# Kernel optimization log

Measured on AMD Instinct MI355X. Metric: run time of the kernel, lower is better.

The kernel has to match this reference:

```python
import jax, jax.numpy as jnp
import numpy as np
from jax import lax

BATCH, CH, SEQ, D_MODEL = 4, 8, 1024, 512
D_STATE, D_CONV, EXPAND = 16, 4, 2
D_INNER = EXPAND * D_MODEL
DT_RANK = (D_MODEL + 15) // 16  # math.ceil(d_model / 16) as in mamba_ssm


def _silu(v):
    return v * jax.nn.sigmoid(v)


def setup_inputs() -> dict:
    key = jax.random.key(0)
    ks = jax.random.split(key, 8)
    s = lambda fan: 1.0 / np.sqrt(fan)
    x = jax.random.normal(ks[0], (BATCH, CH, SEQ, D_MODEL), jnp.float32)
    W_in = jax.random.normal(ks[1], (2 * D_INNER, D_MODEL), jnp.float32) * s(D_MODEL)
    conv_w = jax.random.normal(ks[2], (D_INNER, D_CONV), jnp.float32) * s(D_CONV)
    conv_b = jnp.zeros((D_INNER,), jnp.float32)
    W_xproj = jax.random.normal(ks[3], (DT_RANK + 2 * D_STATE, D_INNER), jnp.float32) * s(D_INNER)
    W_dt = jax.random.normal(ks[4], (D_INNER, DT_RANK), jnp.float32) * s(DT_RANK)
    # dt bias ~ inverse-softplus of dt in [1e-3, 0.1] (mamba init)
    dt0 = jnp.exp(jax.random.uniform(ks[5], (D_INNER,), jnp.float32) * (np.log(0.1) - np.log(1e-3)) + np.log(1e-3))
    b_dt = dt0 + jnp.log(-jnp.expm1(-dt0))
    A_log = jnp.log(jnp.broadcast_to(jnp.arange(1, D_STATE + 1, dtype=jnp.float32), (D_INNER, D_STATE)))
    D = jnp.ones((D_INNER,), jnp.float32)
    W_out = jax.random.normal(ks[6], (D_MODEL, D_INNER), jnp.float32) * s(D_INNER)
    return {"x": x, "W_in": W_in, "conv_w": conv_w, "conv_b": conv_b,
            "W_xproj": W_xproj, "W_dt": W_dt, "b_dt": b_dt,
            "A_log": A_log, "D": D, "W_out": W_out}


def _mamba(u, W_in, conv_w, conv_b, W_xproj, W_dt, b_dt, A_log, D, W_out):
    # u: (B, L, d_model)
    Bn, L, _ = u.shape
    xz = u @ W_in.T                                  # (B, L, 2*d_inner)
    xs, z = jnp.split(xz, 2, axis=-1)
    # depthwise causal conv1d, padding=d_conv-1, truncated to L
    xt = jnp.pad(xs.transpose(0, 2, 1), ((0, 0), (0, 0), (D_CONV - 1, 0)))  # (B, d_inner, L+pad)
    xc = lax.conv_general_dilated(xt, conv_w[:, None, :], (1,), 'VALID',
                                  feature_group_count=D_INNER,
                                  dimension_numbers=('NCH', 'OIH', 'NCH'))   # (B, d_inner, L)
    xs = _silu((xc + conv_b[None, :, None]).transpose(0, 2, 1))              # (B, L, d_inner)
    x_dbl = xs @ W_xproj.T                           # (B, L, dt_rank + 2*d_state)
    dt_in = x_dbl[..., :DT_RANK]
    Bm = x_dbl[..., DT_RANK:DT_RANK + D_STATE]       # (B, L, d_state)
    Cm = x_dbl[..., DT_RANK + D_STATE:]              # (B, L, d_state)
    dt = jax.nn.softplus(dt_in @ W_dt.T + b_dt)      # (B, L, d_inner)
    A = -jnp.exp(A_log)                              # (d_inner, d_state)

    def step(h, inp):
        dt_t, B_t, C_t, x_t = inp                    # (B,di), (B,ds), (B,ds), (B,di)
        dA = jnp.exp(dt_t[..., None] * A)            # (B, di, ds)
        h = dA * h + (dt_t * x_t)[..., None] * B_t[:, None, :]
        y = jnp.einsum('bds,bs->bd', h, C_t)
        return h, y

    h0 = jnp.zeros((Bn, D_INNER, D_STATE), xs.dtype)
    xsL = (dt.transpose(1, 0, 2), Bm.transpose(1, 0, 2), Cm.transpose(1, 0, 2), xs.transpose(1, 0, 2))
    _, ys = lax.scan(step, h0, xsL)                  # ys: (L, B, d_inner)
    y = ys.transpose(1, 0, 2) + xs * D
    y = y * _silu(z)
    return y @ W_out.T                               # (B, L, d_model)


def reference(x, W_in, conv_w, conv_b, W_xproj, W_dt, b_dt, A_log, D, W_out):
    b, c, L, dm = x.shape
    # shared Mamba weights over channels -> fold channel into batch (== per-channel loop)
    u = x.reshape(b * c, L, dm)
    out = _mamba(u, W_in, conv_w, conv_b, W_xproj, W_dt, b_dt, A_log, D, W_out)
    return out.reshape(b, c, L, dm)
```

## Files before the change

kernel.cpp:

```cpp
#include <hip/hip_runtime.h>
#include <hip/hip_bf16.h>
#include <math.h>

#define BATCHN   4
#define CHN      8
#define SEQ      1024
#define DMODEL   512
#define DSTATE   16
#define DCONV    4
#define DINNER   1024
#define DTRANK   32
#define NROWS    32768
#define XD       64
#define NBC      32

#define GCH   16
#define CLEN  (SEQ / GCH)
#define SUB   32
#define PSLOT 17

#define CSPL  8
#define CTS   (SEQ / CSPL)

enum { EPI_NONE = 0, EPI_GATE = 1 };

__device__ __forceinline__ float siluf(float v) {
    return v / (1.0f + expf(-v));
}
__device__ __forceinline__ float softplus_fast(float v) {
    return (v > 20.0f) ? v : __logf(1.0f + __expf(v));
}

typedef short short8 __attribute__((ext_vector_type(8)));
typedef float floatx4 __attribute__((ext_vector_type(4)));

__device__ __forceinline__ unsigned short f2bf_rne(float f) {
    unsigned int u = __float_as_uint(f);
    u += 0x7fffu + ((u >> 16) & 1u);
    return (unsigned short)(u >> 16);
}
__device__ __forceinline__ float bf2f(unsigned short h) {
    return __uint_as_float(((unsigned int)h) << 16);
}

__global__ __launch_bounds__(256)
void split_w(const float* __restrict__ W, unsigned char* __restrict__ W2,
             int R, int K) {
    const int KB = K >> 5;
    const int idx = blockIdx.x * 256 + threadIdx.x;
    if (idx >= R * KB) return;
    const int row = idx / KB;
    const int kb  = idx - row * KB;
    const float* src = W + (size_t)row * K + kb * 32;
    unsigned short h[32], l[32];
#pragma unroll
    for (int e = 0; e < 32; e += 4) {
        const float4 v = *(const float4*)(src + e);
        const float vv[4] = {v.x, v.y, v.z, v.w};
#pragma unroll
        for (int q = 0; q < 4; ++q) {
            const unsigned short hi = f2bf_rne(vv[q]);
            h[e + q] = hi;
            l[e + q] = f2bf_rne(vv[q] - bf2f(hi));
        }
    }
    unsigned char* dst = W2 + ((size_t)row * KB + kb) * 128;
    union { short8 v; unsigned short u[8]; } pk;
#pragma unroll
    for (int c = 0; c < 4; ++c) {
#pragma unroll
        for (int e = 0; e < 8; ++e) pk.u[e] = h[c * 8 + e];
        *(short8*)(dst + c * 16) = pk.v;
    }
#pragma unroll
    for (int c = 0; c < 4; ++c) {
#pragma unroll
        for (int e = 0; e < 8; ++e) pk.u[e] = l[c * 8 + e];
        *(short8*)(dst + 64 + c * 16) = pk.v;
    }
}

template <bool B_PRE, int EPI>
__global__ __launch_bounds__(256, 2)
void gemm_split(const float* __restrict__ A, int lda,
                const float* __restrict__ Bf, const unsigned char* __restrict__ B2,
                int ldb,
                float* __restrict__ C, int ldc,
                int K) {
    __shared__ __align__(16) unsigned short Ah[128][40];
    __shared__ __align__(16) unsigned short Al[128][40];
    __shared__ __align__(16) unsigned short Bh[128][40];
    __shared__ __align__(16) unsigned short Bl[128][40];

    const int tid  = threadIdx.x;
    const int lane = tid & 63;
    const int wv   = tid >> 6;
    const int quad = lane >> 4;
    const int m16  = lane & 15;
    const int wm   = (wv & 1) * 64;
    const int wn   = (wv >> 1) * 64;
    const int m0   = blockIdx.y * 128;
    const int n0   = blockIdx.x * 128;

    const int srow = tid >> 1;
    const int skb  = (tid & 1) * 16;

    const unsigned char* bptr = nullptr;
    if constexpr (B_PRE)
        bptr = B2 + (size_t)(n0 + srow) * (K >> 5) * 128 + 2 * skb;

    floatx4 acc[4][4];
#pragma unroll
    for (int i = 0; i < 4; ++i)
#pragma unroll
        for (int j = 0; j < 4; ++j) acc[i][j] = (floatx4){0.f, 0.f, 0.f, 0.f};

    union U { short8 v; unsigned short u[8]; };

    for (int k0 = 0; k0 < K; k0 += 32) {
        const float* ap = A + (size_t)(m0 + srow) * lda + k0 + skb;
        const float4 a0 = *(const float4*)(ap + 0);
        const float4 a1 = *(const float4*)(ap + 4);
        const float4 a2 = *(const float4*)(ap + 8);
        const float4 a3 = *(const float4*)(ap + 12);
        const float af[16] = {a0.x, a0.y, a0.z, a0.w, a1.x, a1.y, a1.z, a1.w,
                              a2.x, a2.y, a2.z, a2.w, a3.x, a3.y, a3.z, a3.w};

        short8 pb0, pb1, pb2, pb3;
        U bh0, bh1, bl0, bl1;
        if constexpr (B_PRE) {
            pb0 = *(const short8*)(bptr);
            pb1 = *(const short8*)(bptr + 16);
            pb2 = *(const short8*)(bptr + 64);
            pb3 = *(const short8*)(bptr + 80);
            bptr += 128;
        } else {
            const float* bp = Bf + (size_t)(n0 + srow) * ldb + k0 + skb;
            const float4 b0 = *(const float4*)(bp + 0);
            const float4 b1 = *(const float4*)(bp + 4);
            const float4 b2 = *(const float4*)(bp + 8);
            const float4 b3 = *(const float4*)(bp + 12);
            const float bf[16] = {b0.x, b0.y, b0.z, b0.w, b1.x, b1.y, b1.z, b1.w,
                                  b2.x, b2.y, b2.z, b2.w, b3.x, b3.y, b3.z, b3.w};
#pragma unroll
            for (int e = 0; e < 8; ++e) {
                const unsigned short ha = f2bf_rne(bf[e]);
                bh0.u[e] = ha; bl0.u[e] = f2bf_rne(bf[e] - bf2f(ha));
                const unsigned short hb = f2bf_rne(bf[8 + e]);
                bh1.u[e] = hb; bl1.u[e] = f2bf_rne(bf[8 + e] - bf2f(hb));
            }
        }

        U ah0, ah1, al0, al1;
#pragma unroll
        for (int e = 0; e < 8; ++e) {
            const unsigned short ha = f2bf_rne(af[e]);
            ah0.u[e] = ha; al0.u[e] = f2bf_rne(af[e] - bf2f(ha));
            const unsigned short hb = f2bf_rne(af[8 + e]);
            ah1.u[e] = hb; al1.u[e] = f2bf_rne(af[8 + e] - bf2f(hb));
        }

        __syncthreads();
        *(short8*)&Ah[srow][skb]     = ah0.v;
        *(short8*)&Ah[srow][skb + 8] = ah1.v;
        *(short8*)&Al[srow][skb]     = al0.v;
        *(short8*)&Al[srow][skb + 8] = al1.v;
        if constexpr (B_PRE) {
            *(short8*)&Bh[srow][skb]     = pb0;
            *(short8*)&Bh[srow][skb + 8] = pb1;
            *(short8*)&Bl[srow][skb]     = pb2;
            *(short8*)&Bl[srow][skb + 8] = pb3;
        } else {
            *(short8*)&Bh[srow][skb]     = bh0.v;
            *(short8*)&Bh[srow][skb + 8] = bh1.v;
            *(short8*)&Bl[srow][skb]     = bl0.v;
            *(short8*)&Bl[srow][skb + 8] = bl1.v;
        }
        __syncthreads();

        short8 a_h[4], a_l[4], b_h[4], b_l[4];
#pragma unroll
        for (int i = 0; i < 4; ++i) {
            a_h[i] = *(const short8*)&Ah[wm + i * 16 + m16][quad * 8];
            a_l[i] = *(const short8*)&Al[wm + i * 16 + m16][quad * 8];
            b_h[i] = *(const short8*)&Bh[wn + i * 16 + m16][quad * 8];
            b_l[i] = *(const short8*)&Bl[wn + i * 16 + m16][quad * 8];
        }
#pragma unroll
        for (int i = 0; i < 4; ++i)
#pragma unroll
            for (int j = 0; j < 4; ++j) {
                acc[i][j] = __builtin_amdgcn_mfma_f32_16x16x32_bf16(
                    a_h[i], b_h[j], acc[i][j], 0, 0, 0);
                acc[i][j] = __builtin_amdgcn_mfma_f32_16x16x32_bf16(
                    a_l[i], b_h[j], acc[i][j], 0, 0, 0);
                acc[i][j] = __builtin_amdgcn_mfma_f32_16x16x32_bf16(
                    a_h[i], b_l[j], acc[i][j], 0, 0, 0);
            }
    }

#pragma unroll
    for (int i = 0; i < 4; ++i)
#pragma unroll
        for (int j = 0; j < 4; ++j) {
            const int col = n0 + wn + j * 16 + m16;
#pragma unroll
            for (int r = 0; r < 4; ++r) {
                const int row = m0 + wm + i * 16 + quad * 4 + r;
                const size_t off = (size_t)row * ldc + col;
                const float v = acc[i][j][r];
                if (EPI == EPI_NONE) C[off] = v;
                else                 C[off] = C[off] * siluf(v);
            }
        }
}

#define TBM 64
#define TBN 64
#define TBK 16

__global__ __launch_bounds__(256)
void gemm_atb(const float* __restrict__ A, int lda,
              const float* __restrict__ B, int ldb,
              float* __restrict__ C, int ldc,
              int K) {
    __shared__ float As[TBM][TBK + 1];
    __shared__ float Bs[TBN][TBK + 1];

    const int tid = threadIdx.x;
    const int tx = tid & 15;
    const int ty = tid >> 4;
    const int m0 = blockIdx.y * TBM;
    const int n0 = blockIdx.x * TBN;

    const int lr = tid >> 2;
    const int lc = (tid & 3) * 4;

    float acc[4][4];
#pragma unroll
    for (int i = 0; i < 4; ++i)
#pragma unroll
        for (int j = 0; j < 4; ++j) acc[i][j] = 0.0f;

    for (int k0 = 0; k0 < K; k0 += TBK) {
        const float4 av = *(const float4*)(A + (size_t)(m0 + lr) * lda + k0 + lc);
        const float4 bv = *(const float4*)(B + (size_t)(n0 + lr) * ldb + k0 + lc);
        As[lr][lc + 0] = av.x; As[lr][lc + 1] = av.y;
        As[lr][lc + 2] = av.z; As[lr][lc + 3] = av.w;
        Bs[lr][lc + 0] = bv.x; Bs[lr][lc + 1] = bv.y;
        Bs[lr][lc + 2] = bv.z; Bs[lr][lc + 3] = bv.w;
        __syncthreads();

#pragma unroll
        for (int kk = 0; kk < TBK; ++kk) {
            float a[4], b[4];
#pragma unroll
            for (int i = 0; i < 4; ++i) a[i] = As[ty * 4 + i][kk];
#pragma unroll
            for (int j = 0; j < 4; ++j) b[j] = Bs[tx * 4 + j][kk];
#pragma unroll
            for (int i = 0; i < 4; ++i)
#pragma unroll
                for (int j = 0; j < 4; ++j) acc[i][j] += a[i] * b[j];
        }
        __syncthreads();
    }

#pragma unroll
    for (int i = 0; i < 4; ++i) {
        const int r = m0 + ty * 4 + i;
#pragma unroll
        for (int j = 0; j < 4; ++j) {
            const int c = n0 + tx * 4 + j;
            C[(size_t)r * ldc + c] = acc[i][j];
        }
    }
}

__global__ __launch_bounds__(256)
void halo_save(const float* __restrict__ xs, float* __restrict__ halo) {
    const int idx = blockIdx.x * 256 + threadIdx.x;
    if (idx >= NBC * (CSPL - 1) * 3 * DINNER) return;
    const int d  = idx & (DINNER - 1);
    int r = idx >> 10;
    const int j  = r % 3;  r /= 3;
    const int sp = (r % (CSPL - 1)) + 1;
    const int b  = r / (CSPL - 1);
    halo[(((size_t)b * CSPL + sp) * 3 + j) * DINNER + d] =
        xs[((size_t)b * SEQ + sp * CTS - 3 + j) * DINNER + d];
}

__global__ __launch_bounds__(256)
void conv_split_silu(float* __restrict__ xs,
                     const float* __restrict__ conv_w,
                     const float* __restrict__ conv_b,
                     const float* __restrict__ halo) {
    const int gid = blockIdx.x * 256 + threadIdx.x;
    const int d  = gid & (DINNER - 1);
    const int sp = (gid >> 10) & (CSPL - 1);
    const int b  = gid >> 13;
    const float w0 = conv_w[d * DCONV + 0];
    const float w1 = conv_w[d * DCONV + 1];
    const float w2 = conv_w[d * DCONV + 2];
    const float w3 = conv_w[d * DCONV + 3];
    const float cb = conv_b[d];
    float x0, x1, x2;
    if (sp == 0) {
        x0 = 0.0f; x1 = 0.0f; x2 = 0.0f;
    } else {
        const float* hsrc = halo + (((size_t)b * CSPL + sp) * 3) * DINNER + d;
        x0 = hsrc[0];
        x1 = hsrc[DINNER];
        x2 = hsrc[2 * DINNER];
    }
    size_t p = ((size_t)b * SEQ + sp * CTS) * DINNER + d;
    for (int t = 0; t < CTS; ++t, p += DINNER) {
        const float xv = xs[p];
        const float acc = cb + w0 * x0 + w1 * x1 + w2 * x2 + w3 * xv;
        xs[p] = siluf(acc);
        x0 = x1; x1 = x2; x2 = xv;
    }
}

__device__ __forceinline__ size_t ps_idx(int c, int b, int slot, int d) {
    return ((size_t)(c * NBC + b) * PSLOT + slot) * DINNER + d;
}

template <int PASS>
__global__ __launch_bounds__(256)
void scan_chunk_kernel(float* __restrict__ xs,
                       const float* __restrict__ x_dbl,
                       const float* __restrict__ W_dt,
                       const float* __restrict__ b_dt,
                       const float* __restrict__ A_log,
                       const float* __restrict__ Dp,
                       float* __restrict__ ps) {
    const int tid = threadIdx.x;
    const int c  = blockIdx.x & (GCH - 1);
    const int dg = (blockIdx.x >> 4) & 3;
    const int b  = blockIdx.x >> 6;
    const int d  = (dg << 8) + tid;

    if (PASS == 0 && c == GCH - 1) return;

    float wdt[DTRANK];
#pragma unroll
    for (int k = 0; k < DTRANK; ++k) wdt[k] = W_dt[d * DTRANK + k];
    const float bdt = b_dt[d];
    const float Dv = Dp[d];

    float a[DSTATE], h[DSTATE];
    bool afast = true;
#pragma unroll
    for (int s = 0; s < DSTATE; ++s) {
        a[s] = -expf(A_log[d * DSTATE + s]);
        afast = afast && (fabsf(a[s] + (float)(s + 1)) <= 3e-3f * (float)(s + 1));
    }

    float dtsum = 0.0f;
#pragma unroll
    for (int s = 0; s < DSTATE; ++s) h[s] = 0.0f;

    if (PASS == 1) {
        for (int j = 0; j < c; ++j) {
            const float dsj = ps[ps_idx(j, b, 0, d)];
            if (afast) {
                const float F = __expf(dsj * a[0]);
                float P = F;
#pragma unroll
                for (int s = 0; s < DSTATE; ++s) {
                    h[s] = fmaf(P, h[s], ps[ps_idx(j, b, 1 + s, d)]);
                    P *= F;
                }
            } else {
#pragma unroll
                for (int s = 0; s < DSTATE; ++s)
                    h[s] = fmaf(__expf(dsj * a[s]), h[s],
                                ps[ps_idx(j, b, 1 + s, d)]);
            }
        }
    }

    __shared__ float bc[SUB][XD];
    const size_t brow = (size_t)b * SEQ + (size_t)c * CLEN;

    for (int t0 = 0; t0 < CLEN; t0 += SUB) {
        __syncthreads();
        if (PASS == 0) {
            for (int e = tid; e < SUB * 12; e += 256) {
                const int tt = e / 12;
                const int c4 = (e - tt * 12) * 4;
                const float4 v = *(const float4*)(x_dbl + (brow + t0 + tt) * XD + c4);
                bc[tt][c4 + 0] = v.x; bc[tt][c4 + 1] = v.y;
                bc[tt][c4 + 2] = v.z; bc[tt][c4 + 3] = v.w;
            }
        } else {
            for (int e = tid; e < SUB * 16; e += 256) {
                const int tt = e >> 4;
                const int c4 = (e & 15) * 4;
                const float4 v = *(const float4*)(x_dbl + (brow + t0 + tt) * XD + c4);
                bc[tt][c4 + 0] = v.x; bc[tt][c4 + 1] = v.y;
                bc[tt][c4 + 2] = v.z; bc[tt][c4 + 3] = v.w;
            }
        }
        __syncthreads();

        for (int tt = 0; tt < SUB; ++tt) {
            float g0 = 0.0f, g1 = 0.0f, g2 = 0.0f, g3 = 0.0f;
#pragma unroll
            for (int k = 0; k < DTRANK; k += 4) {
                const float4 q = *(const float4*)&bc[tt][k];
                g0 = fmaf(q.x, wdt[k + 0], g0);
                g1 = fmaf(q.y, wdt[k + 1], g1);
                g2 = fmaf(q.z, wdt[k + 2], g2);
                g3 = fmaf(q.w, wdt[k + 3], g3);
            }
            const float dtv = softplus_fast(bdt + ((g0 + g1) + (g2 + g3)));
            if (PASS == 0) dtsum += dtv;

            union F4 { float4 v; float f[4]; };
            F4 Bv[4], Cv[4];
#pragma unroll
            for (int q = 0; q < 4; ++q)
                Bv[q].v = *(const float4*)&bc[tt][DTRANK + q * 4];
            if (PASS == 1) {
#pragma unroll
                for (int q = 0; q < 4; ++q)
                    Cv[q].v = *(const float4*)&bc[tt][DTRANK + DSTATE + q * 4];
            }

            const size_t row = brow + t0 + tt;
            const float xv = xs[row * DINNER + d];
            const float pre = dtv * xv;
            float y0 = 0.0f, y1 = 0.0f;
            if (afast) {
                const float E = __expf(dtv * a[0]);
                float dA = E;
#pragma unroll
                for (int s = 0; s < DSTATE; ++s) {
                    h[s] = fmaf(dA, h[s], pre * Bv[s >> 2].f[s & 3]);
                    if (PASS == 1) {
                        if (s & 1) y1 = fmaf(h[s], Cv[s >> 2].f[s & 3], y1);
                        else       y0 = fmaf(h[s], Cv[s >> 2].f[s & 3], y0);
                    }
                    dA *= E;
                }
            } else {
#pragma unroll
                for (int s = 0; s < DSTATE; ++s) {
                    const float dA = __expf(dtv * a[s]);
                    h[s] = fmaf(dA, h[s], pre * Bv[s >> 2].f[s & 3]);
                    if (PASS == 1) {
                        if (s & 1) y1 = fmaf(h[s], Cv[s >> 2].f[s & 3], y1);
                        else       y0 = fmaf(h[s], Cv[s >> 2].f[s & 3], y0);
                    }
                }
            }
            if (PASS == 1) xs[row * DINNER + d] = fmaf(xv, Dv, y0 + y1);
        }
    }

    if (PASS == 0) {
        ps[ps_idx(c, b, 0, d)] = dtsum;
#pragma unroll
        for (int s = 0; s < DSTATE; ++s)
            ps[ps_idx(c, b, 1 + s, d)] = h[s];
    }
}

extern "C" void kernel_launch(void* const* d_in, const int* in_sizes, int n_in,
                              void* d_out, int out_size, void* d_ws, size_t ws_size,
                              hipStream_t stream) {
    const float* x       = (const float*)d_in[0];
    const float* W_in    = (const float*)d_in[1];
    const float* conv_w  = (const float*)d_in[2];
    const float* conv_b  = (const float*)d_in[3];
    const float* W_xproj = (const float*)d_in[4];
    const float* W_dt    = (const float*)d_in[5];
    const float* b_dt    = (const float*)d_in[6];
    const float* A_log   = (const float*)d_in[7];
    const float* Dp      = (const float*)d_in[8];
    const float* W_out   = (const float*)d_in[9];
    float* out = (float*)d_out;

    float* xs    = (float*)d_ws;
    float* x_dbl = out;
    float* ps    = out + (size_t)NROWS * XD;
    unsigned char* w2in = (unsigned char*)(out + 11534336);
    float* halo  = out + 12582912;

    const size_t xs_bytes = (size_t)NROWS * DINNER * 4;
    unsigned char* w2out = (unsigned char*)d_ws + xs_bytes;
    const bool have_wout = ws_size >= xs_bytes + (size_t)DMODEL * (DINNER / 32) * 128;

    dim3 blk(256);

    split_w<<<(2048 * 16) / 256, blk, 0, stream>>>(W_in, w2in, 2048, DMODEL);
    if (have_wout)
        split_w<<<(512 * 32) / 256, blk, 0, stream>>>(W_out, w2out, DMODEL, DINNER);

    gemm_split<true, EPI_NONE><<<dim3(DINNER / 128, NROWS / 128), blk, 0, stream>>>(
        x, DMODEL, nullptr, w2in, 0, xs, DINNER, DMODEL);

    halo_save<<<(NBC * (CSPL - 1) * 3 * DINNER) / 256, blk, 0, stream>>>(xs, halo);
    conv_split_silu<<<NBC * CSPL * DINNER / 256, blk, 0, stream>>>(
        xs, conv_w, conv_b, halo);

    gemm_atb<<<dim3(XD / TBN, NROWS / TBM), blk, 0, stream>>>(
        xs, DINNER, W_xproj, DINNER, x_dbl, XD, DINNER);

    scan_chunk_kernel<0><<<NBC * 4 * GCH, blk, 0, stream>>>(
        xs, x_dbl, W_dt, b_dt, A_log, Dp, ps);
    scan_chunk_kernel<1><<<NBC * 4 * GCH, blk, 0, stream>>>(
        xs, x_dbl, W_dt, b_dt, A_log, Dp, ps);

    gemm_split<true, EPI_GATE><<<dim3(DINNER / 128, NROWS / 128), blk, 0, stream>>>(
        x, DMODEL, nullptr, w2in + (size_t)1024 * 16 * 128, 0, xs, DINNER, DMODEL);

    if (have_wout)
        gemm_split<true, EPI_NONE><<<dim3(DMODEL / 128, NROWS / 128), blk, 0, stream>>>(
            xs, DINNER, nullptr, w2out, 0, out, DMODEL, DINNER);
    else
        gemm_split<false, EPI_NONE><<<dim3(DMODEL / 128, NROWS / 128), blk, 0, stream>>>(
            xs, DINNER, W_out, nullptr, DINNER, out, DMODEL, DINNER);
}
```

Baseline: 971.9 us.

## Compute dt projection in scan kernel with split-bf16 MFMA instead of scalar FMAs

Inside the chunked scan kernels, the per-timestep 32-wide dt projection (x_dbl dt part times W_dt) moves from per-thread scalar FMAs to MFMA 16x16x32 bf16 instructions. Both operands are split into hi/lo bf16 pairs to keep near-fp32 accuracy, and W_dt is pre-split by an extra split_w launch. Softplus results go into a swizzled shared dt buffer, and the xs column values for a sub-block are prefetched into registers. This cuts VALU work and the 32 W_dt registers per thread, at the cost of extra shared memory, another sync and a small extra launch.

```diff
diff --git a/kernel.cpp b/kernel.cpp
--- a/kernel.cpp
+++ b/kernel.cpp
@@ -330,12 +330,16 @@
 __global__ __launch_bounds__(256)
 void scan_chunk_kernel(float* __restrict__ xs,
                        const float* __restrict__ x_dbl,
-                       const float* __restrict__ W_dt,
+                       const unsigned char* __restrict__ wdt2,
                        const float* __restrict__ b_dt,
                        const float* __restrict__ A_log,
                        const float* __restrict__ Dp,
                        float* __restrict__ ps) {
-    const int tid = threadIdx.x;
+    const int tid  = threadIdx.x;
+    const int lane = tid & 63;
+    const int wv   = tid >> 6;
+    const int quad = lane >> 4;
+    const int m16  = lane & 15;
     const int c  = blockIdx.x & (GCH - 1);
     const int dg = (blockIdx.x >> 4) & 3;
     const int b  = blockIdx.x >> 6;
@@ -343,20 +347,27 @@
 
     if (PASS == 0 && c == GCH - 1) return;
 
-    float wdt[DTRANK];
-#pragma unroll
-    for (int k = 0; k < DTRANK; ++k) wdt[k] = W_dt[d * DTRANK + k];
-    const float bdt = b_dt[d];
+    const int dbase = (dg << 8) + wv * 64;
+    short8 wdh[4], wdl[4];
+    float bdt4[4];
+#pragma unroll
+    for (int q = 0; q < 4; ++q) {
+        const unsigned char* wp = wdt2 + (size_t)(dbase + q * 16 + m16) * 128;
+        wdh[q] = *(const short8*)(wp + quad * 16);
+        wdl[q] = *(const short8*)(wp + 64 + quad * 16);
+        bdt4[q] = b_dt[dbase + q * 16 + m16];
+    }
+
     const float Dv = Dp[d];
-
-    float a[DSTATE], h[DSTATE];
+    const float a0 = -expf(A_log[d * DSTATE]);
     bool afast = true;
 #pragma unroll
     for (int s = 0; s < DSTATE; ++s) {
-        a[s] = -expf(A_log[d * DSTATE + s]);
-        afast = afast && (fabsf(a[s] + (float)(s + 1)) <= 3e-3f * (float)(s + 1));
-    }
-
+        const float as = -expf(A_log[d * DSTATE + s]);
+        afast = afast && (fabsf(as + (float)(s + 1)) <= 3e-3f * (float)(s + 1));
+    }
+
+    float h[DSTATE];
     float dtsum = 0.0f;
 #pragma unroll
     for (int s = 0; s < DSTATE; ++s) h[s] = 0.0f;
@@ -365,7 +376,7 @@
         for (int j = 0; j < c; ++j) {
             const float dsj = ps[ps_idx(j, b, 0, d)];
             if (afast) {
-                const float F = __expf(dsj * a[0]);
+                const float F = __expf(dsj * a0);
                 float P = F;
 #pragma unroll
                 for (int s = 0; s < DSTATE; ++s) {
@@ -374,67 +385,92 @@
                 }
             } else {
 #pragma unroll
-                for (int s = 0; s < DSTATE; ++s)
-                    h[s] = fmaf(__expf(dsj * a[s]), h[s],
+                for (int s = 0; s < DSTATE; ++s) {
+                    const float as = -expf(A_log[d * DSTATE + s]);
+                    h[s] = fmaf(__expf(dsj * as), h[s],
                                 ps[ps_idx(j, b, 1 + s, d)]);
-            }
-        }
-    }
-
-    __shared__ float bc[SUB][XD];
+                }
+            }
+        }
+    }
+
+    __shared__ float          bcf[SUB][32];
+    __shared__ unsigned short bch[SUB][32];
+    __shared__ unsigned short bcl[SUB][32];
+    __shared__ float          dt_s[SUB][256];
+
     const size_t brow = (size_t)b * SEQ + (size_t)c * CLEN;
 
     for (int t0 = 0; t0 < CLEN; t0 += SUB) {
         __syncthreads();
-        if (PASS == 0) {
-            for (int e = tid; e < SUB * 12; e += 256) {
-                const int tt = e / 12;
-                const int c4 = (e - tt * 12) * 4;
-                const float4 v = *(const float4*)(x_dbl + (brow + t0 + tt) * XD + c4);
-                bc[tt][c4 + 0] = v.x; bc[tt][c4 + 1] = v.y;
-                bc[tt][c4 + 2] = v.z; bc[tt][c4 + 3] = v.w;
-            }
-        } else {
-            for (int e = tid; e < SUB * 16; e += 256) {
-                const int tt = e >> 4;
-                const int c4 = (e & 15) * 4;
-                const float4 v = *(const float4*)(x_dbl + (brow + t0 + tt) * XD + c4);
-                bc[tt][c4 + 0] = v.x; bc[tt][c4 + 1] = v.y;
-                bc[tt][c4 + 2] = v.z; bc[tt][c4 + 3] = v.w;
-            }
-        }
-        __syncthreads();
-
+        constexpr int NF4 = (PASS == 0) ? 12 : 16;
+        for (int e = tid; e < SUB * NF4; e += 256) {
+            const int tt = e / NF4;
+            const int cc = (e - tt * NF4) * 4;
+            const float4 v = *(const float4*)(x_dbl + (brow + t0 + tt) * XD + cc);
+            if (cc < 32) {
+                const float vv[4] = {v.x, v.y, v.z, v.w};
+#pragma unroll
+                for (int q = 0; q < 4; ++q) {
+                    const unsigned short hi = f2bf_rne(vv[q]);
+                    bch[tt][cc + q] = hi;
+                    bcl[tt][cc + q] = f2bf_rne(vv[q] - bf2f(hi));
+                }
+            } else {
+                *(float4*)&bcf[tt][cc - 32] = v;
+            }
+        }
+        __syncthreads();
+
+        float xr[SUB];
+        {
+            const float* xp = xs + (brow + t0) * DINNER + d;
+#pragma unroll
+            for (int e = 0; e < SUB; ++e) xr[e] = xp[(size_t)e * DINNER];
+        }
+
+#pragma unroll
+        for (int tb = 0; tb < 2; ++tb) {
+            const short8 ah = *(const short8*)&bch[tb * 16 + m16][quad * 8];
+            const short8 al = *(const short8*)&bcl[tb * 16 + m16][quad * 8];
+#pragma unroll
+            for (int q = 0; q < 4; ++q) {
+                floatx4 acc = (floatx4){0.f, 0.f, 0.f, 0.f};
+                acc = __builtin_amdgcn_mfma_f32_16x16x32_bf16(ah, wdh[q], acc, 0, 0, 0);
+                acc = __builtin_amdgcn_mfma_f32_16x16x32_bf16(al, wdh[q], acc, 0, 0, 0);
+                acc = __builtin_amdgcn_mfma_f32_16x16x32_bf16(ah, wdl[q], acc, 0, 0, 0);
+                const int colbase = (wv * 64 + q * 16 + m16) ^ ((quad & 1) << 4);
+#pragma unroll
+                for (int r = 0; r < 4; ++r) {
+                    const float dtv = softplus_fast(acc[r] + bdt4[q]);
+                    dt_s[tb * 16 + quad * 4 + r][colbase] = dtv;
+                }
+            }
+        }
+        __syncthreads();
+
+        float* xw = xs + (brow + t0) * DINNER + d;
+#pragma unroll
         for (int tt = 0; tt < SUB; ++tt) {
-            float g0 = 0.0f, g1 = 0.0f, g2 = 0.0f, g3 = 0.0f;
-#pragma unroll
-            for (int k = 0; k < DTRANK; k += 4) {
-                const float4 q = *(const float4*)&bc[tt][k];
-                g0 = fmaf(q.x, wdt[k + 0], g0);
-                g1 = fmaf(q.y, wdt[k + 1], g1);
-                g2 = fmaf(q.z, wdt[k + 2], g2);
-                g3 = fmaf(q.w, wdt[k + 3], g3);
-            }
-            const float dtv = softplus_fast(bdt + ((g0 + g1) + (g2 + g3)));
+            const float dtv = dt_s[tt][tid ^ (((tt >> 2) & 1) << 4)];
             if (PASS == 0) dtsum += dtv;
 
             union F4 { float4 v; float f[4]; };
             F4 Bv[4], Cv[4];
 #pragma unroll
             for (int q = 0; q < 4; ++q)
-                Bv[q].v = *(const float4*)&bc[tt][DTRANK + q * 4];
+                Bv[q].v = *(const float4*)&bcf[tt][q * 4];
             if (PASS == 1) {
 #pragma unroll
                 for (int q = 0; q < 4; ++q)
-                    Cv[q].v = *(const float4*)&bc[tt][DTRANK + DSTATE + q * 4];
-            }
-
-            const size_t row = brow + t0 + tt;
-            const float xv = xs[row * DINNER + d];
+                    Cv[q].v = *(const float4*)&bcf[tt][16 + q * 4];
+            }
+
+            const float xv = xr[tt];
             const float pre = dtv * xv;
             float y0 = 0.0f, y1 = 0.0f;
             if (afast) {
-                const float E = __expf(dtv * a[0]);
+                const float E = __expf(dtv * a0);
                 float dA = E;
 #pragma unroll
                 for (int s = 0; s < DSTATE; ++s) {
@@ -448,7 +484,8 @@
             } else {
 #pragma unroll
                 for (int s = 0; s < DSTATE; ++s) {
-                    const float dA = __expf(dtv * a[s]);
+                    const float as = -expf(A_log[d * DSTATE + s]);
+                    const float dA = __expf(dtv * as);
                     h[s] = fmaf(dA, h[s], pre * Bv[s >> 2].f[s & 3]);
                     if (PASS == 1) {
                         if (s & 1) y1 = fmaf(h[s], Cv[s >> 2].f[s & 3], y1);
@@ -456,7 +493,7 @@
                     }
                 }
             }
-            if (PASS == 1) xs[row * DINNER + d] = fmaf(xv, Dv, y0 + y1);
+            if (PASS == 1) xw[(size_t)tt * DINNER] = fmaf(xv, Dv, y0 + y1);
         }
     }
 
@@ -488,6 +525,7 @@
     float* ps    = out + (size_t)NROWS * XD;
     unsigned char* w2in = (unsigned char*)(out + 11534336);
     float* halo  = out + 12582912;
+    unsigned char* wdt2 = (unsigned char*)(out + 13893632);
 
     const size_t xs_bytes = (size_t)NROWS * DINNER * 4;
     unsigned char* w2out = (unsigned char*)d_ws + xs_bytes;
@@ -496,6 +534,7 @@
     dim3 blk(256);
 
     split_w<<<(2048 * 16) / 256, blk, 0, stream>>>(W_in, w2in, 2048, DMODEL);
+    split_w<<<(1024 * 1 + 255) / 256, blk, 0, stream>>>(W_dt, wdt2, DINNER, DTRANK);
     if (have_wout)
         split_w<<<(512 * 32) / 256, blk, 0, stream>>>(W_out, w2out, DMODEL, DINNER);
 
@@ -510,9 +549,9 @@
         xs, DINNER, W_xproj, DINNER, x_dbl, XD, DINNER);
 
     scan_chunk_kernel<0><<<NBC * 4 * GCH, blk, 0, stream>>>(
-        xs, x_dbl, W_dt, b_dt, A_log, Dp, ps);
+        xs, x_dbl, wdt2, b_dt, A_log, Dp, ps);
     scan_chunk_kernel<1><<<NBC * 4 * GCH, blk, 0, stream>>>(
-        xs, x_dbl, W_dt, b_dt, A_log, Dp, ps);
+        xs, x_dbl, wdt2, b_dt, A_log, Dp, ps);
 
     gemm_split<true, EPI_GATE><<<dim3(DINNER / 128, NROWS / 128), blk, 0, stream>>>(
         x, DMODEL, nullptr, w2in + (size_t)1024 * 16 * 128, 0, xs, DINNER, DMODEL);
```

New measurement: 1.056 ms. 8.7% more time.
